# Kernel optimization log

Hardware: AMD Instinct MI355X
Metric: run time of the kernel (lower is better)

Reference implementation:

```python
import jax, jax.numpy as jnp
import numpy as np

H = 768        # bert hidden_size
HID = 512      # lstm_hidden
HALF = HID // 2
T = 20         # tagset_size
START, STOP = 18, 19
S = 16386      # input positions incl. CLS/SEP
NEG = -10000.0


def setup_inputs() -> dict:
    key = jax.random.key(0)
    ks = jax.random.split(key, 12)
    sc_x = 1.0
    x = jax.random.normal(ks[0], (1, S, H), dtype=jnp.float32)
    # PyTorch LSTM params (gate order i,f,g,o), one layer, bidirectional
    s_ih = 1.0 / np.sqrt(HALF)
    w_ih_f = jax.random.uniform(ks[1], (4 * HALF, H), jnp.float32, -s_ih, s_ih)
    w_hh_f = jax.random.uniform(ks[2], (4 * HALF, HALF), jnp.float32, -s_ih, s_ih)
    b_ih_f = jax.random.uniform(ks[3], (4 * HALF,), jnp.float32, -s_ih, s_ih)
    b_hh_f = jax.random.uniform(ks[4], (4 * HALF,), jnp.float32, -s_ih, s_ih)
    w_ih_b = jax.random.uniform(ks[5], (4 * HALF, H), jnp.float32, -s_ih, s_ih)
    w_hh_b = jax.random.uniform(ks[6], (4 * HALF, HALF), jnp.float32, -s_ih, s_ih)
    b_ih_b = jax.random.uniform(ks[7], (4 * HALF,), jnp.float32, -s_ih, s_ih)
    b_hh_b = jax.random.uniform(ks[8], (4 * HALF,), jnp.float32, -s_ih, s_ih)
    s_t = 1.0 / np.sqrt(HID)
    w_tag = jax.random.uniform(ks[9], (T, HID), jnp.float32, -s_t, s_t)
    b_tag = jax.random.uniform(ks[10], (T,), jnp.float32, -s_t, s_t)
    transitions = jax.random.normal(ks[11], (T, T), dtype=jnp.float32)
    transitions = transitions.at[START, :].set(NEG).at[:, STOP].set(NEG)
    return {
        "x": x,
        "w_ih_f": w_ih_f, "w_hh_f": w_hh_f, "b_ih_f": b_ih_f, "b_hh_f": b_hh_f,
        "w_ih_b": w_ih_b, "w_hh_b": w_hh_b, "b_ih_b": b_ih_b, "b_hh_b": b_hh_b,
        "w_tag": w_tag, "b_tag": b_tag, "transitions": transitions,
    }


def _lstm_one_step(xt, w_ih, b_ih, b_hh):
    # Original passes [1, N, H] to a batch_first=False LSTM => seq_len=1,
    # batch=N, zero initial state. So each token does ONE cell step:
    # h0=c0=0 => hh contribution is only b_hh.
    g = xt @ w_ih.T + b_ih + b_hh          # [N, 4*HALF]
    i, f, gg, o = jnp.split(g, 4, axis=-1)  # PyTorch gate order i,f,g,o
    c = jax.nn.sigmoid(i) * jnp.tanh(gg)    # f*c0 = 0
    return jax.nn.sigmoid(o) * jnp.tanh(c)  # [N, HALF]


def reference(x, w_ih_f, w_hh_f, b_ih_f, b_hh_f,
              w_ih_b, w_hh_b, b_ih_b, b_hh_b,
              w_tag, b_tag, transitions):
    tok = x[0, 1:-1, :]                     # narrow(1,1,S-2): drop CLS/SEP -> [N,H]
    h_f = _lstm_one_step(tok, w_ih_f, b_ih_f, b_hh_f)
    h_b = _lstm_one_step(tok, w_ih_b, b_ih_b, b_hh_b)
    enc = jnp.concatenate([h_f, h_b], axis=-1)   # [N, HID]
    feats = enc @ w_tag.T + b_tag                # [N, T] emission scores

    # ---- Viterbi decode (sequential DP over tokens) ----
    init = jnp.full((T,), NEG, dtype=feats.dtype).at[START].set(0.0)

    def vstep(fv, feat):
        scores = fv[None, :] + transitions       # [next_tag, prev_tag]
        bp = jnp.argmax(scores, axis=1)          # backpointers [T]
        fv_new = jnp.max(scores, axis=1) + feat
        return fv_new, bp

    fv, bps = jax.lax.scan(vstep, init, feats)   # bps: [N, T]
    terminal = fv + transitions[STOP]
    best = jnp.argmax(terminal)
    path_score = terminal[best]

    def btrack(b, bp):
        return bp[b], b                          # emit tag at time t, move to t-1

    _, best_path = jax.lax.scan(btrack, best, bps, reverse=True)  # [N] in time order
    return path_score, best_path
```

## Files before the change

kernel.cpp:

```cpp
#include <hip/hip_runtime.h>
#include <math.h>

#define HDIM 768
#define HIDD 512
#define NTOK 16384
#define NT 20
#define CHUNKS 128
#define CLEN 128

typedef unsigned short ushort_t;
typedef __attribute__((ext_vector_type(8))) short bf16x8;
typedef __attribute__((ext_vector_type(4))) float f32x4;

__device__ __forceinline__ float sigm(float x){ return 1.0f/(1.0f+expf(-x)); }

__device__ __forceinline__ ushort_t f2bf(float f){
    unsigned int u = __float_as_uint(f);
    unsigned int r = (u + 0x7fffu + ((u >> 16) & 1u)) >> 16;
    return (ushort_t)r;
}
__device__ __forceinline__ float bf2f(ushort_t b){
    return __uint_as_float(((unsigned int)b) << 16);
}

#define GLD16(gp, lp) __builtin_amdgcn_global_load_lds( \
    (const __attribute__((address_space(1))) void*)(gp), \
    (__attribute__((address_space(3))) void*)(lp), 16, 0, 0)

__global__ __launch_bounds__(256) void conv_kernel(
    const float* __restrict__ x,
    const float* __restrict__ wf, const float* __restrict__ wb,
    ushort_t* __restrict__ Ah, ushort_t* __restrict__ Al,
    ushort_t* __restrict__ Bh, ushort_t* __restrict__ Bl)
{
    const int bid = blockIdx.x;
    if (bid < 1152){
        int t = bid*256 + threadIdx.x;
        int n = t / 192, c4 = (t - n*192)*4;
        int dir = n / 768, nr = n - dir*768;
        int gate = nr >> 8, j = nr & 255;
        int wrow = j + ((gate==0)?0:((gate==1)?512:768));
        const float* src = dir ? wb : wf;
        const float4 v = *(const float4*)(src + (size_t)wrow*HDIM + c4);
        float f[4] = {v.x, v.y, v.z, v.w};
        ushort_t h[4], l[4];
        #pragma unroll
        for (int i=0;i<4;++i){
            h[i] = f2bf(f[i]);
            l[i] = f2bf(f[i] - bf2f(h[i]));
        }
        *(ushort4*)(Bh + (size_t)n*HDIM + c4) = make_ushort4(h[0],h[1],h[2],h[3]);
        *(ushort4*)(Bl + (size_t)n*HDIM + c4) = make_ushort4(l[0],l[1],l[2],l[3]);
    } else {
        int t = (bid-1152)*256 + threadIdx.x;
        int row = t / 192, c4 = (t - row*192)*4;
        const float4 v = *(const float4*)(x + (size_t)(row+1)*HDIM + c4);
        float f[4] = {v.x, v.y, v.z, v.w};
        ushort_t h[4], l[4];
        #pragma unroll
        for (int i=0;i<4;++i){
            h[i] = f2bf(f[i]);
            l[i] = f2bf(f[i] - bf2f(h[i]));
        }
        *(ushort4*)(Ah + (size_t)row*HDIM + c4) = make_ushort4(h[0],h[1],h[2],h[3]);
        *(ushort4*)(Al + (size_t)row*HDIM + c4) = make_ushort4(l[0],l[1],l[2],l[3]);
    }
}

#define VMCNT(n) asm volatile("s_waitcnt vmcnt(" #n ")" ::: "memory")
#define BARRIER() asm volatile("s_barrier" ::: "memory")

#define READ_BG(g, bb) do{                                                    \
    bfr[g][0] = *(const bf16x8*)((bb) + (g)*8192 + boffB[0]);                 \
    bfr[g][1] = *(const bf16x8*)((bb) + (g)*8192 + 4096 + boffB[0]);          \
    bfr[g][2] = *(const bf16x8*)((bb) + (g)*8192 + boffB[1]);                 \
    bfr[g][3] = *(const bf16x8*)((bb) + (g)*8192 + 4096 + boffB[1]);          \
}while(0)

#define READ_A(S, ab) do{ _Pragma("unroll") for (int f=0; f<4; ++f){          \
    aH##S[f] = *(const bf16x8*)((ab) + aoffB[f]);                             \
    aL##S[f] = *(const bf16x8*)((ab) + 8192 + aoffB[f]); } }while(0)

#define MFMA_CLUSTER(g, S) do{                                                \
  __builtin_amdgcn_s_setprio(1);                                              \
  _Pragma("unroll")                                                           \
  for (int fn=0; fn<2; ++fn){                                                 \
    _Pragma("unroll")                                                         \
    for (int fm=0; fm<4; ++fm){                                               \
      acc[g][fm][fn] = __builtin_amdgcn_mfma_f32_16x16x32_bf16(aH##S[fm],     \
          bfr[g][fn*2], acc[g][fm][fn], 0, 0, 0);                             \
      acc[g][fm][fn] = __builtin_amdgcn_mfma_f32_16x16x32_bf16(aL##S[fm],     \
          bfr[g][fn*2], acc[g][fm][fn], 0, 0, 0);                             \
      acc[g][fm][fn] = __builtin_amdgcn_mfma_f32_16x16x32_bf16(aH##S[fm],     \
          bfr[g][fn*2+1], acc[g][fm][fn], 0, 0, 0);                           \
    }                                                                         \
  }                                                                           \
  __builtin_amdgcn_s_setprio(0);                                              \
}while(0)

#define KT_BODY(kt, P, CUR, NXT) do{                                          \
    const int k0n = ((kt)+1)*32;                                              \
    char* abn = smem + (1-(P))*16384;                                         \
    char* bbn = smem + 32768 + (1-(P))*24576;                                 \
    const char* bbc = smem + 32768 + (P)*24576;                               \
                  \
    GLD16(Ah + aoff0 + k0n, abn + wbB);                                       \
    GLD16(Ah + aoff1 + k0n, abn + 4096 + wbB);                                \
    GLD16(Al + aoff0 + k0n, abn + 8192 + wbB);                                \
    GLD16(Al + aoff1 + k0n, abn + 12288 + wbB);                               \
    GLD16(Bh + bOff[0] + k0n, bbn + wbB);                                     \
    GLD16(Bl + bOff[0] + k0n, bbn + 4096 + wbB);                              \
    VMCNT(8); BARRIER();                                                      \
    READ_BG(1, bbc);                                                          \
    MFMA_CLUSTER(0, CUR);                                                     \
                  \
    GLD16(Bh + bOff[1] + k0n, bbn + 8192 + wbB);                              \
    GLD16(Bl + bOff[1] + k0n, bbn + 12288 + wbB);                             \
    VMCNT(8); BARRIER();                                                      \
    READ_BG(2, bbc);                                                          \
    MFMA_CLUSTER(1, CUR);                                                     \
              \
    GLD16(Bh + bOff[2] + k0n, bbn + 16384 + wbB);                             \
    GLD16(Bl + bOff[2] + k0n, bbn + 20480 + wbB);                             \
    VMCNT(4); BARRIER();                                                      \
    READ_A(NXT, abn);                                                         \
    READ_BG(0, bbn);                                                          \
    MFMA_CLUSTER(2, CUR);                                                     \
}while(0)

__global__ __launch_bounds__(256, 2) void gemm_fused(
    const ushort_t* __restrict__ Ah, const ushort_t* __restrict__ Al,
    const ushort_t* __restrict__ Bh, const ushort_t* __restrict__ Bl,
    const float* __restrict__ bihf, const float* __restrict__ bhhf,
    const float* __restrict__ bihb, const float* __restrict__ bhhb,
    const float* __restrict__ wtag, float* __restrict__ featsp)
{
    __shared__ __align__(16) char smem[81920];
    float* hbuf = (float*)smem;
    float* wts  = (float*)(smem + 16640);

    const int tid = threadIdx.x;
    const int bx = blockIdx.x;
    const int xcd = bx & 7, g3 = bx >> 3;
    const int q = g3 & 7, mt = (g3 >> 3)*8 + xcd;
    const int dir = q >> 2, j0 = (q & 3)*64;
    const int row0 = mt*128;
    const float* __restrict__ bih = dir ? bihb : bihf;
    const float* __restrict__ bhh = dir ? bhhb : bhhf;

    const int lane = tid & 63, wv = tid >> 6;
    const int wm = wv >> 1, wn = wv & 1;
    const int lm = lane & 15, lq = lane >> 4;
    const int wbB = (tid & 192) * 16;

    const int P_ = tid >> 3, s_ = tid & 7;
    const int q_ = s_ ^ (P_ & 7);
    const int mA = (P_ << 1) | (q_ >> 2);
    const int k8s = q_ & 3;
    const size_t aoff0 = (size_t)(row0 + mA)*HDIM + k8s*8;
    const size_t aoff1 = (size_t)(row0 + 64 + mA)*HDIM + k8s*8;
    size_t bOff[3];
    #pragma unroll
    for (int g=0; g<3; ++g)
        bOff[g] = (size_t)(dir*768 + g*256 + j0 + mA)*HDIM + k8s*8;

    int aoffB[4], boffB[2];
    #pragma unroll
    for (int f=0; f<4; ++f){
        int m = wm*64 + f*16 + lm;
        int rg = m >> 6, r = m & 63;
        aoffB[f] = rg*4096 + ((r>>1)*8 + ((((r&1)<<2)|lq) ^ ((r>>1)&7)))*16;
    }
    #pragma unroll
    for (int f=0; f<2; ++f){
        int n = wn*32 + f*16 + lm;
        boffB[f] = ((n>>1)*8 + ((((n&1)<<2)|lq) ^ ((n>>1)&7)))*16;
    }

    f32x4 acc[3][4][2];
    #pragma unroll
    for (int g=0; g<3; ++g)
        #pragma unroll
        for (int fm=0; fm<4; ++fm)
            #pragma unroll
            for (int fn=0; fn<2; ++fn)
                acc[g][fm][fn] = (f32x4){0.f,0.f,0.f,0.f};

    bf16x8 aH0[4], aL0[4], aH1[4], aL1[4];
    bf16x8 bfr[3][4];

    {
        char* ab = smem;
        char* bb = smem + 32768;
        GLD16(Ah + aoff0, ab + wbB);
        GLD16(Ah + aoff1, ab + 4096 + wbB);
        GLD16(Al + aoff0, ab + 8192 + wbB);
        GLD16(Al + aoff1, ab + 12288 + wbB);
        GLD16(Bh + bOff[0], bb + wbB);
        GLD16(Bl + bOff[0], bb + 4096 + wbB);
        GLD16(Bh + bOff[1], bb + 8192 + wbB);
        GLD16(Bl + bOff[1], bb + 12288 + wbB);
        GLD16(Bh + bOff[2], bb + 16384 + wbB);
        GLD16(Bl + bOff[2], bb + 20480 + wbB);
        VMCNT(4); BARRIER();
        READ_A(0, (const char*)smem);
        READ_BG(0, (const char*)(smem + 32768));
    }

    #pragma unroll 1
    for (int kt2 = 0; kt2 < 11; ++kt2){
        const int kt = kt2*2;
        KT_BODY(kt,   0, 0, 1);
        KT_BODY(kt+1, 1, 1, 0);
    }
    KT_BODY(22, 0, 0, 1);

    {
        const char* bbc = smem + 32768 + 24576;
        VMCNT(2); BARRIER();
        READ_BG(1, bbc);
        MFMA_CLUSTER(0, 1);
        VMCNT(0); BARRIER();
        READ_BG(2, bbc);
        MFMA_CLUSTER(1, 1);
        MFMA_CLUSTER(2, 1);
    }

    int jcol[2];
    #pragma unroll
    for (int f=0; f<2; ++f) jcol[f] = j0 + wn*32 + f*16 + lm;

    float bi[2], bg_[2], bo[2];
    #pragma unroll
    for (int f=0; f<2; ++f){
        bi[f]  = bih[jcol[f]]       + bhh[jcol[f]];
        bg_[f] = bih[512 + jcol[f]] + bhh[512 + jcol[f]];
        bo[f]  = bih[768 + jcol[f]] + bhh[768 + jcol[f]];
    }
    float hv[4][2][4];
    #pragma unroll
    for (int fm=0; fm<4; ++fm)
        #pragma unroll
        for (int fn=0; fn<2; ++fn)
            #pragma unroll
            for (int r=0; r<4; ++r){
                float cv = sigm(acc[0][fm][fn][r] + bi[fn]) *
                           tanhf(acc[1][fm][fn][r] + bg_[fn]);
                hv[fm][fn][r] = sigm(acc[2][fm][fn][r] + bo[fn]) * tanhf(cv);
            }

    __syncthreads();
    for (int i2=tid; i2<NT*64; i2+=256){
        int t = i2 >> 6, j = i2 & 63;
        wts[i2] = wtag[t*HIDD + dir*256 + j0 + j];
    }
    float* fq = featsp + (size_t)q * (NTOK*NT);
    #pragma unroll 1
    for (int ph=0; ph<2; ++ph){
        __syncthreads();
        if (wm == ph){
            #pragma unroll
            for (int fm=0; fm<4; ++fm)
                #pragma unroll
                for (int fn=0; fn<2; ++fn)
                    #pragma unroll
                    for (int r=0; r<4; ++r){
                        int mloc = fm*16 + lq*4 + r;
                        int jloc = wn*32 + fn*16 + lm;
                        hbuf[mloc*65 + jloc] = hv[fm][fn][r];
                    }
        }
        __syncthreads();
        const int mrow = tid & 63, grp = tid >> 6;
        const int tg0 = grp*5;
        float s[5] = {0.f,0.f,0.f,0.f,0.f};
        for (int j=0;j<64;++j){
            float h = hbuf[mrow*65 + j];
            #pragma unroll
            for (int tt=0; tt<5; ++tt)
                s[tt] = fmaf(h, wts[(tg0+tt)*64 + j], s[tt]);
        }
        const int mglob = row0 + ph*64 + mrow;
        #pragma unroll
        for (int tt=0; tt<5; ++tt)
            fq[(size_t)mglob*NT + tg0 + tt] = s[tt];
    }
}

__device__ __forceinline__ void load_fl(
    const float* __restrict__ featsp, const float* __restrict__ btg,
    float* fl, int c, int tid, int nthr)
{
    const int base = c*(CLEN*NT/4);
    for (int idx=tid; idx<CLEN*NT/4; idx+=nthr){
        float4 s[8];
        #pragma unroll
        for (int p=0; p<8; ++p)
            s[p] = ((const float4*)(featsp + (size_t)p*NTOK*NT))[base+idx];
        float4 v;
        v.x = ((s[0].x+s[1].x)+(s[2].x+s[3].x)) + ((s[4].x+s[5].x)+(s[6].x+s[7].x));
        v.y = ((s[0].y+s[1].y)+(s[2].y+s[3].y)) + ((s[4].y+s[5].y)+(s[6].y+s[7].y));
        v.z = ((s[0].z+s[1].z)+(s[2].z+s[3].z)) + ((s[4].z+s[5].z)+(s[6].z+s[7].z));
        v.w = ((s[0].w+s[1].w)+(s[2].w+s[3].w)) + ((s[4].w+s[5].w)+(s[6].w+s[7].w));
        int t0 = (idx*4) % 20;
        v.x += btg[t0]; v.y += btg[t0+1]; v.z += btg[t0+2]; v.w += btg[t0+3];
        ((float4*)fl)[idx] = v;
    }
}

__global__ __launch_bounds__(512) void vit_chunkmat(
    const float* __restrict__ featsp, const float* __restrict__ btag,
    const float* __restrict__ trans, float* __restrict__ Pall)
{
    __shared__ float fl[CLEN*NT];
    __shared__ float Pb[2][NT*NT];
    const int c = blockIdx.x, tid = threadIdx.x;
    load_fl(featsp, btag, fl, c, tid, 512);
    const bool act = tid < NT*NT;
    const int i = tid/20, j = tid - i*20;
    float tr[NT];
    if (act){
        #pragma unroll
        for (int k=0;k<NT;++k) tr[k] = trans[i*NT+k];
        Pb[0][tid] = (i==j) ? 0.f : -1e30f;
    }
    __syncthreads();
    int cur = 0;
    for (int t=0;t<CLEN;++t){
        float m = -3.0e38f;
        if (act){
            #pragma unroll
            for (int k=0;k<NT;++k) m = fmaxf(m, tr[k] + Pb[cur][k*NT+j]);
            m += fl[t*NT+i];
            Pb[cur^1][tid] = m;
        }
        __syncthreads();
        cur ^= 1;
    }
    if (act) Pall[(size_t)c*(NT*NT) + tid] = Pb[cur][tid];
}

__global__ __launch_bounds__(128) void vit_scan(
    const float* __restrict__ Pall, const float* __restrict__ trans,
    float* __restrict__ fvstart, float* __restrict__ dout, int* __restrict__ bestws)
{
    __shared__ float Pb[NT*NT];
    __shared__ float fv[NT];
    const int tid = threadIdx.x;
    float4 pn = {0.f,0.f,0.f,0.f};
    if (tid<100) pn = ((const float4*)Pall)[tid];
    if (tid<NT) fv[tid] = (tid==18) ? 0.f : -10000.f;
    for (int c=0;c<CHUNKS;++c){
        if (tid<100) ((float4*)Pb)[tid] = pn;
        if (tid<100 && c+1<CHUNKS) pn = ((const float4*)(Pall + (size_t)(c+1)*(NT*NT)))[tid];
        __syncthreads();
        if (tid<NT) fvstart[c*NT+tid] = fv[tid];
        float nf = -3.0e38f;
        if (tid<NT){
            #pragma unroll
            for (int j=0;j<NT;++j) nf = fmaxf(nf, Pb[tid*NT+j] + fv[j]);
        }
        __syncthreads();
        if (tid<NT) fv[tid] = nf;
    }
    __syncthreads();
    if (tid==0){
        float best = -3.0e38f; int bidx = 0;
        for (int j=0;j<NT;++j){
            float tv = fv[j] + trans[19*NT+j];
            if (tv > best){ best = tv; bidx = j; }
        }
        dout[0] = best;
        bestws[0] = bidx;
    }
}

__global__ __launch_bounds__(128) void vit_replay(
    const float* __restrict__ featsp, const float* __restrict__ btag,
    const float* __restrict__ trans, const float* __restrict__ fvstart,
    unsigned int* __restrict__ bpout, int* __restrict__ Hout)
{
    __shared__ float fl[CLEN*NT];
    __shared__ float fv[NT];
    __shared__ unsigned char bp[CLEN*NT];
    const int c = blockIdx.x, tid = threadIdx.x;
    load_fl(featsp, btag, fl, c, tid, 128);
    float tr[NT];
    if (tid<NT){
        fv[tid] = fvstart[c*NT+tid];
        #pragma unroll
        for (int k=0;k<NT;++k) tr[k] = trans[tid*NT+k];
    }
    __syncthreads();
    for (int t=0;t<CLEN;++t){
        float best = 0.f; int bj = 0;
        if (tid<NT){
            best = tr[0] + fv[0];
            #pragma unroll
            for (int j=1;j<NT;++j){
                float v = tr[j] + fv[j];
                if (v > best){ best = v; bj = j; }
            }
        }
        __syncthreads();
        if (tid<NT){
            fv[tid] = best + fl[t*NT+tid];
            bp[t*NT+tid] = (unsigned char)bj;
        }
        __syncthreads();
    }
    for (int idx=tid; idx<CLEN*NT/4; idx+=128)
        bpout[(size_t)c*(CLEN*NT/4) + idx] = ((unsigned int*)bp)[idx];
    if (tid<NT){
        int m = tid;
        for (int t=CLEN-1;t>=0;--t) m = bp[t*NT+m];
        Hout[c*NT+tid] = m;
    }
}

__global__ __launch_bounds__(64) void bt_fill(
    const unsigned int* __restrict__ bpin, const int* __restrict__ Hin,
    const int* __restrict__ bestws, float* __restrict__ dout)
{
    __shared__ int Hl[CHUNKS*NT];
    __shared__ unsigned char bp[CLEN*NT];
    __shared__ float ob[CLEN];
    const int c = blockIdx.x, tid = threadIdx.x;
    for (int idx=tid; idx<CHUNKS*NT; idx+=64) Hl[idx] = Hin[idx];
    for (int idx=tid; idx<CLEN*NT/4; idx+=64)
        ((unsigned int*)bp)[idx] = bpin[(size_t)c*(CLEN*NT/4) + idx];
    __syncthreads();
    if (tid==0){
        int e = bestws[0];
        for (int cc=CHUNKS-1; cc>c; --cc) e = Hl[cc*NT+e];
        for (int t=CLEN-1;t>=0;--t){ ob[t] = (float)e; e = bp[t*NT+e]; }
    }
    __syncthreads();
    for (int idx=tid; idx<CLEN; idx+=64)
        dout[1 + c*CLEN + idx] = ob[idx];
}

extern "C" void kernel_launch(void* const* d_in, const int* in_sizes, int n_in,
                              void* d_out, int out_size, void* d_ws, size_t ws_size,
                              hipStream_t stream)
{
    const float* x    = (const float*)d_in[0];
    const float* wf   = (const float*)d_in[1];
    const float* bihf = (const float*)d_in[3];
    const float* bhhf = (const float*)d_in[4];
    const float* wb   = (const float*)d_in[5];
    const float* bihb = (const float*)d_in[7];
    const float* bhhb = (const float*)d_in[8];
    const float* wtag = (const float*)d_in[9];
    const float* btag = (const float*)d_in[10];
    const float* trans= (const float*)d_in[11];
    float* out = (float*)d_out;

    char* w = (char*)d_ws;
    ushort_t* Ah = (ushort_t*)w;         w += 25165824;
    ushort_t* Al = (ushort_t*)w;         w += 25165824;
    ushort_t* Bh = (ushort_t*)w;         w += 2359296;
    ushort_t* Bl = (ushort_t*)w;         w += 2359296;
    float* featsp = (float*)w;           w += 10485760;
    float* Pall  = (float*)w;            w += 204800;
    float* fvst  = (float*)w;            w += 10240;
    int* Hmap    = (int*)w;              w += 10240;
    unsigned int* bp = (unsigned int*)w; w += 327680;
    int* best    = (int*)w;

    conv_kernel<<<13440, 256, 0, stream>>>(x, wf, wb, Ah, Al, Bh, Bl);
    gemm_fused<<<1024, 256, 0, stream>>>(Ah, Al, Bh, Bl, bihf, bhhf, bihb, bhhb,
                                         wtag, featsp);
    vit_chunkmat<<<CHUNKS, 512, 0, stream>>>(featsp, btag, trans, Pall);
    vit_scan<<<1, 128, 0, stream>>>(Pall, trans, fvst, out, best);
    vit_replay<<<CHUNKS, 128, 0, stream>>>(featsp, btag, trans, fvst, bp, Hmap);
    bt_fill<<<CHUNKS, 64, 0, stream>>>(bp, Hmap, best, out);
}
```

Before: 372.3 us.

## Widen GEMM tile to 128 gate columns with 512-thread blocks and unified smem stages

The fused LSTM-gate GEMM now uses 512-thread blocks covering 128 rows by 128 hidden columns per gate, up from 64 columns. Each A tile is therefore reused across twice as many outputs, halving A global traffic. The pipeline is split into three phases with explicit lgkmcnt waits and sched barriers. The epilogue is reworked to write four partial feature slabs per block. This raises shared memory to 128KB, which likely limits occupancy to one block per CU, and the explicit waits may serialize LDS reads with MFMA.

```diff
diff --git a/kernel.cpp b/kernel.cpp
--- a/kernel.cpp
+++ b/kernel.cpp
@@ -69,17 +69,20 @@
 
 #define VMCNT(n) asm volatile("s_waitcnt vmcnt(" #n ")" ::: "memory")
 #define BARRIER() asm volatile("s_barrier" ::: "memory")
-
-#define READ_BG(g, bb) do{                                                    \
-    bfr[g][0] = *(const bf16x8*)((bb) + (g)*8192 + boffB[0]);                 \
-    bfr[g][1] = *(const bf16x8*)((bb) + (g)*8192 + 4096 + boffB[0]);          \
-    bfr[g][2] = *(const bf16x8*)((bb) + (g)*8192 + boffB[1]);                 \
-    bfr[g][3] = *(const bf16x8*)((bb) + (g)*8192 + 4096 + boffB[1]);          \
+#define LGKM0()  do{ asm volatile("s_waitcnt lgkmcnt(0)" ::: "memory"); \
+                     __builtin_amdgcn_sched_barrier(0); }while(0)
+
+#define READ_B(g, ab) do{                                                     \
+    bfr[0] = *(const bf16x8*)((ab) + 16384 + (g)*16384 + boffB[0]);           \
+    bfr[1] = *(const bf16x8*)((ab) + 16384 + (g)*16384 + 8192 + boffB[0]);    \
+    bfr[2] = *(const bf16x8*)((ab) + 16384 + (g)*16384 + boffB[1]);           \
+    bfr[3] = *(const bf16x8*)((ab) + 16384 + (g)*16384 + 8192 + boffB[1]);    \
 }while(0)
 
-#define READ_A(S, ab) do{ _Pragma("unroll") for (int f=0; f<4; ++f){          \
-    aH##S[f] = *(const bf16x8*)((ab) + aoffB[f]);                             \
-    aL##S[f] = *(const bf16x8*)((ab) + 8192 + aoffB[f]); } }while(0)
+#define READ_AH(S, ab) do{ _Pragma("unroll") for (int f=0; f<4; ++f)          \
+    aH##S[f] = *(const bf16x8*)((ab) + aoffB[f]); }while(0)
+#define READ_AL(ab) do{ _Pragma("unroll") for (int f=0; f<4; ++f)             \
+    aL[f] = *(const bf16x8*)((ab) + 8192 + aoffB[f]); }while(0)
 
 #define MFMA_CLUSTER(g, S) do{                                                \
   __builtin_amdgcn_s_setprio(1);                                              \
@@ -88,81 +91,91 @@
     _Pragma("unroll")                                                         \
     for (int fm=0; fm<4; ++fm){                                               \
       acc[g][fm][fn] = __builtin_amdgcn_mfma_f32_16x16x32_bf16(aH##S[fm],     \
-          bfr[g][fn*2], acc[g][fm][fn], 0, 0, 0);                             \
-      acc[g][fm][fn] = __builtin_amdgcn_mfma_f32_16x16x32_bf16(aL##S[fm],     \
-          bfr[g][fn*2], acc[g][fm][fn], 0, 0, 0);                             \
+          bfr[fn*2], acc[g][fm][fn], 0, 0, 0);                                \
+      acc[g][fm][fn] = __builtin_amdgcn_mfma_f32_16x16x32_bf16(aL[fm],        \
+          bfr[fn*2], acc[g][fm][fn], 0, 0, 0);                                \
       acc[g][fm][fn] = __builtin_amdgcn_mfma_f32_16x16x32_bf16(aH##S[fm],     \
-          bfr[g][fn*2+1], acc[g][fm][fn], 0, 0, 0);                           \
+          bfr[fn*2+1], acc[g][fm][fn], 0, 0, 0);                              \
     }                                                                         \
   }                                                                           \
   __builtin_amdgcn_s_setprio(0);                                              \
+  __builtin_amdgcn_sched_barrier(0);                                          \
 }while(0)
 
-#define KT_BODY(kt, P, CUR, NXT) do{                                          \
+#define PH0(kt, P, CUR) do{                                                   \
     const int k0n = ((kt)+1)*32;                                              \
-    char* abn = smem + (1-(P))*16384;                                         \
-    char* bbn = smem + 32768 + (1-(P))*24576;                                 \
-    const char* bbc = smem + 32768 + (P)*24576;                               \
-                  \
-    GLD16(Ah + aoff0 + k0n, abn + wbB);                                       \
-    GLD16(Ah + aoff1 + k0n, abn + 4096 + wbB);                                \
-    GLD16(Al + aoff0 + k0n, abn + 8192 + wbB);                                \
-    GLD16(Al + aoff1 + k0n, abn + 12288 + wbB);                               \
-    GLD16(Bh + bOff[0] + k0n, bbn + wbB);                                     \
-    GLD16(Bl + bOff[0] + k0n, bbn + 4096 + wbB);                              \
+    char* abn = smem + (1-(P))*65536;                                         \
+    GLD16(Ah + gA + k0n, abn + wbB);                                          \
+    GLD16(Al + gA + k0n, abn + 8192 + wbB);                                   \
+    GLD16(Bh + gB0 + k0n, abn + 16384 + wbB);                                 \
+    GLD16(Bl + gB0 + k0n, abn + 24576 + wbB);                                 \
     VMCNT(8); BARRIER();                                                      \
-    READ_BG(1, bbc);                                                          \
+    const char* ab = smem + (P)*65536;                                        \
+    READ_AL(ab);                                                              \
+    READ_B(0, ab);                                                            \
+    LGKM0();                                                                  \
     MFMA_CLUSTER(0, CUR);                                                     \
-                  \
-    GLD16(Bh + bOff[1] + k0n, bbn + 8192 + wbB);                              \
-    GLD16(Bl + bOff[1] + k0n, bbn + 12288 + wbB);                             \
+}while(0)
+
+#define PH1(kt, P, CUR) do{                                                   \
+    const int k0n = ((kt)+1)*32;                                              \
+    char* abn = smem + (1-(P))*65536;                                         \
+    GLD16(Bh + gB1 + k0n, abn + 32768 + wbB);                                 \
+    GLD16(Bl + gB1 + k0n, abn + 40960 + wbB);                                 \
     VMCNT(8); BARRIER();                                                      \
-    READ_BG(2, bbc);                                                          \
+    const char* ab = smem + (P)*65536;                                        \
+    READ_B(1, ab);                                                            \
+    LGKM0();                                                                  \
     MFMA_CLUSTER(1, CUR);                                                     \
-              \
-    GLD16(Bh + bOff[2] + k0n, bbn + 16384 + wbB);                             \
-    GLD16(Bl + bOff[2] + k0n, bbn + 20480 + wbB);                             \
+}while(0)
+
+#define PH2(kt, P, CUR, NXT) do{                                              \
+    const int k0n = ((kt)+1)*32;                                              \
+    char* abn = smem + (1-(P))*65536;                                         \
+    GLD16(Bh + gB2 + k0n, abn + 49152 + wbB);                                 \
+    GLD16(Bl + gB2 + k0n, abn + 57344 + wbB);                                 \
     VMCNT(4); BARRIER();                                                      \
-    READ_A(NXT, abn);                                                         \
-    READ_BG(0, bbn);                                                          \
+    const char* ab = smem + (P)*65536;                                        \
+    READ_B(2, ab);                                                            \
+    READ_AH(NXT, abn);                                                        \
+    LGKM0();                                                                  \
     MFMA_CLUSTER(2, CUR);                                                     \
 }while(0)
 
-__global__ __launch_bounds__(256, 2) void gemm_fused(
+__global__ __launch_bounds__(512, 2) void gemm_fused(
     const ushort_t* __restrict__ Ah, const ushort_t* __restrict__ Al,
     const ushort_t* __restrict__ Bh, const ushort_t* __restrict__ Bl,
     const float* __restrict__ bihf, const float* __restrict__ bhhf,
     const float* __restrict__ bihb, const float* __restrict__ bhhb,
     const float* __restrict__ wtag, float* __restrict__ featsp)
 {
-    __shared__ __align__(16) char smem[81920];
+    __shared__ __align__(16) char smem[131072];
     float* hbuf = (float*)smem;
-    float* wts  = (float*)(smem + 16640);
+    float* wts  = (float*)(smem + 33280);
 
     const int tid = threadIdx.x;
     const int bx = blockIdx.x;
     const int xcd = bx & 7, g3 = bx >> 3;
-    const int q = g3 & 7, mt = (g3 >> 3)*8 + xcd;
-    const int dir = q >> 2, j0 = (q & 3)*64;
+    const int qb = g3 & 3, mt = (g3 >> 2)*8 + xcd;
+    const int dir = qb >> 1, jhalf = qb & 1;
+    const int j0 = jhalf*128;
     const int row0 = mt*128;
     const float* __restrict__ bih = dir ? bihb : bihf;
     const float* __restrict__ bhh = dir ? bhhb : bhhf;
 
     const int lane = tid & 63, wv = tid >> 6;
-    const int wm = wv >> 1, wn = wv & 1;
+    const int wm = wv >> 2, wn = wv & 3;
     const int lm = lane & 15, lq = lane >> 4;
-    const int wbB = (tid & 192) * 16;
+    const int wbB = (tid & 448) * 16;
 
     const int P_ = tid >> 3, s_ = tid & 7;
     const int q_ = s_ ^ (P_ & 7);
     const int mA = (P_ << 1) | (q_ >> 2);
     const int k8s = q_ & 3;
-    const size_t aoff0 = (size_t)(row0 + mA)*HDIM + k8s*8;
-    const size_t aoff1 = (size_t)(row0 + 64 + mA)*HDIM + k8s*8;
-    size_t bOff[3];
-    #pragma unroll
-    for (int g=0; g<3; ++g)
-        bOff[g] = (size_t)(dir*768 + g*256 + j0 + mA)*HDIM + k8s*8;
+    const size_t gA  = (size_t)(row0 + mA)*HDIM + k8s*8;
+    const size_t gB0 = (size_t)(dir*768 +           j0 + mA)*HDIM + k8s*8;
+    const size_t gB1 = (size_t)(dir*768 + 256 +     j0 + mA)*HDIM + k8s*8;
+    const size_t gB2 = (size_t)(dir*768 + 512 +     j0 + mA)*HDIM + k8s*8;
 
     int aoffB[4], boffB[2];
     #pragma unroll
@@ -174,7 +187,8 @@
     #pragma unroll
     for (int f=0; f<2; ++f){
         int n = wn*32 + f*16 + lm;
-        boffB[f] = ((n>>1)*8 + ((((n&1)<<2)|lq) ^ ((n>>1)&7)))*16;
+        int rg = n >> 6, r = n & 63;
+        boffB[f] = rg*4096 + ((r>>1)*8 + ((((r&1)<<2)|lq) ^ ((r>>1)&7)))*16;
     }
 
     f32x4 acc[3][4][2];
@@ -186,43 +200,44 @@
             for (int fn=0; fn<2; ++fn)
                 acc[g][fm][fn] = (f32x4){0.f,0.f,0.f,0.f};
 
-    bf16x8 aH0[4], aL0[4], aH1[4], aL1[4];
-    bf16x8 bfr[3][4];
+    bf16x8 aH0[4], aH1[4], aL[4];
+    bf16x8 bfr[4];
 
     {
-        char* ab = smem;
-        char* bb = smem + 32768;
-        GLD16(Ah + aoff0, ab + wbB);
-        GLD16(Ah + aoff1, ab + 4096 + wbB);
-        GLD16(Al + aoff0, ab + 8192 + wbB);
-        GLD16(Al + aoff1, ab + 12288 + wbB);
-        GLD16(Bh + bOff[0], bb + wbB);
-        GLD16(Bl + bOff[0], bb + 4096 + wbB);
-        GLD16(Bh + bOff[1], bb + 8192 + wbB);
-        GLD16(Bl + bOff[1], bb + 12288 + wbB);
-        GLD16(Bh + bOff[2], bb + 16384 + wbB);
-        GLD16(Bl + bOff[2], bb + 20480 + wbB);
+        GLD16(Ah + gA, smem + wbB);
+        GLD16(Al + gA, smem + 8192 + wbB);
+        GLD16(Bh + gB0, smem + 16384 + wbB);
+        GLD16(Bl + gB0, smem + 24576 + wbB);
+        GLD16(Bh + gB1, smem + 32768 + wbB);
+        GLD16(Bl + gB1, smem + 40960 + wbB);
+        GLD16(Bh + gB2, smem + 49152 + wbB);
+        GLD16(Bl + gB2, smem + 57344 + wbB);
         VMCNT(4); BARRIER();
-        READ_A(0, (const char*)smem);
-        READ_BG(0, (const char*)(smem + 32768));
+        READ_AH(0, (const char*)smem);
     }
 
     #pragma unroll 1
     for (int kt2 = 0; kt2 < 11; ++kt2){
         const int kt = kt2*2;
-        KT_BODY(kt,   0, 0, 1);
-        KT_BODY(kt+1, 1, 1, 0);
-    }
-    KT_BODY(22, 0, 0, 1);
+        PH0(kt,   0, 0); PH1(kt,   0, 0); PH2(kt,   0, 0, 1);
+        PH0(kt+1, 1, 1); PH1(kt+1, 1, 1); PH2(kt+1, 1, 1, 0);
+    }
+    PH0(22, 0, 0); PH1(22, 0, 0); PH2(22, 0, 0, 1);
 
     {
-        const char* bbc = smem + 32768 + 24576;
+        const char* ab = smem + 65536;
+        VMCNT(4); BARRIER();
+        READ_AL(ab);
+        READ_B(0, ab);
+        LGKM0();
+        MFMA_CLUSTER(0, 1);
         VMCNT(2); BARRIER();
-        READ_BG(1, bbc);
-        MFMA_CLUSTER(0, 1);
+        READ_B(1, ab);
+        LGKM0();
+        MFMA_CLUSTER(1, 1);
         VMCNT(0); BARRIER();
-        READ_BG(2, bbc);
-        MFMA_CLUSTER(1, 1);
+        READ_B(2, ab);
+        LGKM0();
         MFMA_CLUSTER(2, 1);
     }
 
@@ -250,37 +265,40 @@
             }
 
     __syncthreads();
-    for (int i2=tid; i2<NT*64; i2+=256){
-        int t = i2 >> 6, j = i2 & 63;
-        wts[i2] = wtag[t*HIDD + dir*256 + j0 + j];
-    }
-    float* fq = featsp + (size_t)q * (NTOK*NT);
+    for (int idx=tid; idx<2*NT*64; idx+=512){
+        int cc = idx / (NT*64), r = idx - cc*(NT*64);
+        int t = r >> 6, j = r & 63;
+        wts[idx] = wtag[t*HIDD + dir*256 + j0 + cc*64 + j];
+    }
     #pragma unroll 1
-    for (int ph=0; ph<2; ++ph){
-        __syncthreads();
-        if (wm == ph){
+    for (int cc=0; cc<2; ++cc){
+        __syncthreads();
+        if ((wn >> 1) == cc){
             #pragma unroll
             for (int fm=0; fm<4; ++fm)
                 #pragma unroll
                 for (int fn=0; fn<2; ++fn)
                     #pragma unroll
                     for (int r=0; r<4; ++r){
-                        int mloc = fm*16 + lq*4 + r;
-                        int jloc = wn*32 + fn*16 + lm;
+                        int mloc = wm*64 + fm*16 + lq*4 + r;
+                        int jloc = (wn&1)*32 + fn*16 + lm;
                         hbuf[mloc*65 + jloc] = hv[fm][fn][r];
                     }
         }
         __syncthreads();
-        const int mrow = tid & 63, grp = tid >> 6;
+        const int mrow = tid & 127, grp = tid >> 7;
         const int tg0 = grp*5;
+        const float* wc = wts + cc*(NT*64);
         float s[5] = {0.f,0.f,0.f,0.f,0.f};
         for (int j=0;j<64;++j){
             float h = hbuf[mrow*65 + j];
             #pragma unroll
             for (int tt=0; tt<5; ++tt)
-                s[tt] = fmaf(h, wts[(tg0+tt)*64 + j], s[tt]);
-        }
-        const int mglob = row0 + ph*64 + mrow;
+                s[tt] = fmaf(h, wc[(tg0+tt)*64 + j], s[tt]);
+        }
+        const int p = dir*4 + jhalf*2 + cc;
+        float* fq = featsp + (size_t)p * (NTOK*NT);
+        const int mglob = row0 + mrow;
         #pragma unroll
         for (int tt=0; tt<5; ++tt)
             fq[(size_t)mglob*NT + tg0 + tt] = s[tt];
@@ -469,8 +487,8 @@
     int* best    = (int*)w;
 
     conv_kernel<<<13440, 256, 0, stream>>>(x, wf, wb, Ah, Al, Bh, Bl);
-    gemm_fused<<<1024, 256, 0, stream>>>(Ah, Al, Bh, Bl, bihf, bhhf, bihb, bhhb,
-                                         wtag, featsp);
+    gemm_fused<<<512, 512, 0, stream>>>(Ah, Al, Bh, Bl, bihf, bhhf, bihb, bhhb,
+                                        wtag, featsp);
     vit_chunkmat<<<CHUNKS, 512, 0, stream>>>(featsp, btag, trans, Pall);
     vit_scan<<<1, 128, 0, stream>>>(Pall, trans, fvst, out, best);
     vit_replay<<<CHUNKS, 128, 0, stream>>>(featsp, btag, trans, fvst, bp, Hmap);
```

Result: no change. 370.9 us (-0.4%).
